# Performance work log

Hardware: AMD Instinct MI355X
Metric: run time of the kernel (lower is better)

The kernel has to match this reference:

```python
import jax, jax.numpy as jnp
import numpy as np

T = 10       # Newton-Schulz iterations (module init arg)
EPS = 1e-05  # ridge added to covariance


def setup_inputs() -> dict:
    key = jax.random.key(0)
    # [B, C, H, W] feature map fed into the concept-whitening layer
    X = jax.random.normal(key, (128, 256, 28, 28), dtype=jnp.float32)
    return {"X": X}


def _iternorm_whiten(X):
    """Training-mode IterNorm whitening (g=1 group): ZCA via Newton-Schulz."""
    B, C, H, W = X.shape
    # X.transpose(0,1).view(C, -1): channels-first flatten -> [C, m], m = B*H*W
    x = jnp.moveaxis(X, 0, 1).reshape(C, -1)
    m = x.shape[-1]
    mean = x.mean(-1, keepdims=True)                      # [C, 1]
    xc = x - mean                                         # [C, m]
    I = jnp.eye(C, dtype=X.dtype)
    # Sigma = eps*I + (1/m) * xc @ xc^T
    Sigma = EPS * I + (xc @ xc.T) * (1.0 / m)             # [C, C]
    rTr = 1.0 / jnp.trace(Sigma)                          # scalar
    Sigma_N = Sigma * rTr                                 # trace-normalized

    def newton_step(P, _):
        # P_{k+1} = 1.5*P_k - 0.5 * P_k^3 @ Sigma_N
        P3 = P @ P @ P
        return 1.5 * P - 0.5 * (P3 @ Sigma_N), None

    P, _ = jax.lax.scan(newton_step, I, None, length=T)
    wm = P * jnp.sqrt(rTr)                                # whitening matrix [C, C]
    xn = wm @ xc                                          # [C, m]
    # reshape back: view(C, B, H, W).transpose(0, 1) -> [B, C, H, W]
    return jnp.moveaxis(xn.reshape(C, B, H, W), 0, 1)


def reference(X):
    # IterNormRotation.forward with mode=-1 (default): X_hat = IterNorm.apply(X, ...)
    # The concept-alignment branch (mode >= 0) runs under no_grad and is skipped.
    return _iternorm_whiten(X)
```

## Files before the change

kernel.cpp:

```cpp
#include <hip/hip_runtime.h>


#define HW 784
#define BHW 200704
#define INV_M (1.0f/100352.0f)
#define EPS_RIDGE 1e-5f

typedef __bf16 bf8 __attribute__((ext_vector_type(8)));
typedef float  f4  __attribute__((ext_vector_type(4)));

__device__ __forceinline__ f4 mfma16(bf8 a, bf8 b, f4 c){
  return __builtin_amdgcn_mfma_f32_16x16x32_bf16(a, b, c, 0, 0, 0);
}

__device__ __forceinline__ unsigned short f2bf_rne(float f){
  unsigned u = __builtin_bit_cast(unsigned, f);
  return (unsigned short)((u + 0x7fffu + ((u >> 16) & 1u)) >> 16);
}
__device__ __forceinline__ float bf2f(unsigned short h){
  unsigned u = ((unsigned)h) << 16;
  return __builtin_bit_cast(float, u);
}
__device__ __forceinline__ void split_bf(float f, unsigned short& h, unsigned short& l){
  h = f2bf_rne(f);
  float r = f - bf2f(h);
  l = f2bf_rne(r);
}

__global__ __launch_bounds__(512, 2) void cov_kernel(const float* __restrict__ X,
                                                     float* __restrict__ part,
                                                     float* __restrict__ chansum){
  __shared__ unsigned short Ah[256][40];
  __shared__ unsigned short Al[256][40];
  __shared__ float ssum[256];
  const int t = threadIdx.x;
  const int blk = blockIdx.x;
  const int b = blk >> 1;
  const int h = blk & 1;
  const int base_hw = h * 400;
  const int len    = h ? 384 : 400;
  const int nsteps = h ? 12  : 13;
  const float* __restrict__ Xb = X + (size_t)b * BHW;

  if (t < 256) ssum[t] = 0.0f;

  const int lane = t & 63;
  const int wave = t >> 6;
  const int wm = wave >> 2;
  const int wn = wave & 3;
  const int lr = lane & 15;
  const int ko = lane >> 4;

  f4 acc[8][4];
  #pragma unroll
  for (int m = 0; m < 8; m++)
    #pragma unroll
    for (int n = 0; n < 4; n++) acc[m][n] = f4{0.f, 0.f, 0.f, 0.f};

  float csum[4] = {0.f, 0.f, 0.f, 0.f};
  const int srow = t >> 3;
  const int sfq  = t & 7;

  for (int ks = 0; ks < nsteps; ++ks){
    if (ks) __syncthreads();
    #pragma unroll
    for (int i = 0; i < 4; i++){
      int row = srow + i * 64;
      int hwl = ks * 32 + sfq * 4;
      float4 v = make_float4(0.f, 0.f, 0.f, 0.f);
      if (hwl < len) v = *(const float4*)&Xb[(size_t)row * HW + base_hw + hwl];
      csum[i] += v.x + v.y + v.z + v.w;
      unsigned short h0,l0,h1,l1,h2,l2,h3,l3;
      split_bf(v.x, h0, l0); split_bf(v.y, h1, l1);
      split_bf(v.z, h2, l2); split_bf(v.w, h3, l3);
      *(ushort4*)&Ah[row][sfq * 4] = make_ushort4(h0, h1, h2, h3);
      *(ushort4*)&Al[row][sfq * 4] = make_ushort4(l0, l1, l2, l3);
    }
    __syncthreads();
    bf8 bhf[4], blf[4];
    #pragma unroll
    for (int n = 0; n < 4; n++){
      int coln = wn * 64 + n * 16 + lr;
      bhf[n] = *(const bf8*)&Ah[coln][ko * 8];
      blf[n] = *(const bf8*)&Al[coln][ko * 8];
    }
    #pragma unroll
    for (int m = 0; m < 8; m++){
      int rowm = wm * 128 + m * 16 + lr;
      bf8 ahf = *(const bf8*)&Ah[rowm][ko * 8];
      bf8 alf = *(const bf8*)&Al[rowm][ko * 8];
      #pragma unroll
      for (int n = 0; n < 4; n++){
        acc[m][n] = mfma16(ahf, bhf[n], acc[m][n]);
        acc[m][n] = mfma16(ahf, blf[n], acc[m][n]);
        acc[m][n] = mfma16(alf, bhf[n], acc[m][n]);
      }
    }
  }
  atomicAdd(&ssum[srow      ], csum[0]);
  atomicAdd(&ssum[srow +  64], csum[1]);
  atomicAdd(&ssum[srow + 128], csum[2]);
  atomicAdd(&ssum[srow + 192], csum[3]);
  __syncthreads();
  if (t < 256) atomicAdd(&chansum[t], ssum[t]);

  float* __restrict__ Pp = part + (size_t)blk * 65536;
  const int cr4 = (lane >> 4) * 4;
  #pragma unroll
  for (int m = 0; m < 8; m++){
    #pragma unroll
    for (int n = 0; n < 4; n++){
      int colw = wn * 64 + n * 16 + lr;
      #pragma unroll
      for (int r = 0; r < 4; r++){
        int roww = wm * 128 + m * 16 + cr4 + r;
        Pp[roww * 256 + colw] = acc[m][n][r];
      }
    }
  }
}

__global__ __launch_bounds__(256) void reduce_kernel(const float* __restrict__ part,
                                                     const float* __restrict__ chansum,
                                                     float* __restrict__ Sig,
                                                     float* __restrict__ trace){
  const int i = blockIdx.x;
  const int j = threadIdx.x;
  float s = 0.f;
  #pragma unroll 8
  for (int p = 0; p < 256; p++) s += part[(size_t)p * 65536 + i * 256 + j];
  float mi = chansum[i] * INV_M;
  float mj = chansum[j] * INV_M;
  float v = s * INV_M - mi * mj + ((i == j) ? EPS_RIDGE : 0.f);
  Sig[i * 256 + j] = v;
  if (i == j) atomicAdd(trace, v);
}

__global__ __launch_bounds__(256) void prep_kernel(const float* __restrict__ Sig,
                                                   const float* __restrict__ trace,
                                                   float* __restrict__ SigN,
                                                   float* __restrict__ P1){
  const int idx = blockIdx.x * 256 + threadIdx.x;
  const float rTr = 1.0f / trace[0];
  const float sn = Sig[idx] * rTr;
  SigN[idx] = sn;
  const int i = idx >> 8, j = idx & 255;
  P1[idx] = ((i == j) ? 1.5f : 0.0f) - 0.5f * sn;
}

__global__ __launch_bounds__(256) void ns64_kernel(const float* __restrict__ A,
                                                   const float* __restrict__ B0,
                                                   const float* __restrict__ B1,
                                                   float* __restrict__ O0,
                                                   float* __restrict__ O1,
                                                   const float* __restrict__ E,
                                                   float alpha, float beta){
  const float* __restrict__ B = blockIdx.z ? B1 : B0;
  float* __restrict__ O = blockIdx.z ? O1 : O0;
  __shared__ unsigned short Ah[64][136], Al[64][136], Bh[64][136], Bl[64][136];
  const int t = threadIdx.x;
  const int lane = t & 63;
  const int wave = t >> 6;
  const int wm = wave >> 1, wn = wave & 1;
  const int lr = lane & 15, ko = lane >> 4;
  const int r0 = blockIdx.x * 64, c0 = blockIdx.y * 64;
  const int srow = t >> 2;
  const int sc0 = (t & 3) * 32;
  f4 acc[2][2];
  acc[0][0] = f4{0.f,0.f,0.f,0.f}; acc[0][1] = f4{0.f,0.f,0.f,0.f};
  acc[1][0] = f4{0.f,0.f,0.f,0.f}; acc[1][1] = f4{0.f,0.f,0.f,0.f};

  for (int kh = 0; kh < 2; ++kh){
    if (kh) __syncthreads();
    #pragma unroll
    for (int i = 0; i < 8; i++){
      int col = sc0 + i * 4;
      int gcol = kh * 128 + col;
      unsigned short h0,l0,h1,l1,h2,l2,h3,l3;
      float4 va = *(const float4*)&A[(r0 + srow) * 256 + gcol];
      split_bf(va.x,h0,l0); split_bf(va.y,h1,l1); split_bf(va.z,h2,l2); split_bf(va.w,h3,l3);
      *(ushort4*)&Ah[srow][col] = make_ushort4(h0,h1,h2,h3);
      *(ushort4*)&Al[srow][col] = make_ushort4(l0,l1,l2,l3);
      float4 vb = *(const float4*)&B[(c0 + srow) * 256 + gcol];
      split_bf(vb.x,h0,l0); split_bf(vb.y,h1,l1); split_bf(vb.z,h2,l2); split_bf(vb.w,h3,l3);
      *(ushort4*)&Bh[srow][col] = make_ushort4(h0,h1,h2,h3);
      *(ushort4*)&Bl[srow][col] = make_ushort4(l0,l1,l2,l3);
    }
    __syncthreads();
    #pragma unroll
    for (int ks = 0; ks < 4; ++ks){
      #pragma unroll
      for (int m = 0; m < 2; m++){
        bf8 ahf = *(const bf8*)&Ah[wm * 32 + m * 16 + lr][ks * 32 + ko * 8];
        bf8 alf = *(const bf8*)&Al[wm * 32 + m * 16 + lr][ks * 32 + ko * 8];
        #pragma unroll
        for (int n = 0; n < 2; n++){
          bf8 bhf = *(const bf8*)&Bh[wn * 32 + n * 16 + lr][ks * 32 + ko * 8];
          bf8 blf = *(const bf8*)&Bl[wn * 32 + n * 16 + lr][ks * 32 + ko * 8];
          acc[m][n] = mfma16(ahf, bhf, acc[m][n]);
          acc[m][n] = mfma16(ahf, blf, acc[m][n]);
          acc[m][n] = mfma16(alf, bhf, acc[m][n]);
        }
      }
    }
  }
  const int cr4 = (lane >> 4) * 4;
  #pragma unroll
  for (int m = 0; m < 2; m++)
    #pragma unroll
    for (int n = 0; n < 2; n++)
      #pragma unroll
      for (int r = 0; r < 4; r++){
        int row = r0 + wm * 32 + m * 16 + cr4 + r;
        int col = c0 + wn * 32 + n * 16 + lr;
        float v = alpha * acc[m][n][r];
        if (beta != 0.0f) v += beta * E[row * 256 + col];
        O[row * 256 + col] = v;
      }
}

__global__ __launch_bounds__(256) void wmprep_kernel(const float* __restrict__ P,
                                                     const float* __restrict__ trace,
                                                     const float* __restrict__ chansum,
                                                     unsigned short* __restrict__ wmhi,
                                                     unsigned short* __restrict__ wmlo,
                                                     float* __restrict__ woff){
  const int i = blockIdx.x, t = threadIdx.x;
  __shared__ float red[256];
  const float s = sqrtf(1.0f / trace[0]);
  float v = P[i * 256 + t] * s;
  unsigned short h, l;
  split_bf(v, h, l);
  wmhi[i * 256 + t] = h;
  wmlo[i * 256 + t] = l;
  red[t] = v * (chansum[t] * INV_M);
  __syncthreads();
  for (int st = 128; st > 0; st >>= 1){
    if (t < st) red[t] += red[t + st];
    __syncthreads();
  }
  if (t == 0) woff[i] = red[0];
}

__global__ __launch_bounds__(512, 2) void whiten_kernel(const float* __restrict__ X,
                                                        const unsigned short* __restrict__ wmhi,
                                                        const unsigned short* __restrict__ wmlo,
                                                        const float* __restrict__ woff,
                                                        float* __restrict__ out){
  __shared__ unsigned short Ahs[256][40], Als[256][40];
  __shared__ unsigned short Bhs[112][40], Bls[112][40];
  const int blk = blockIdx.x;
  const int b = blk / 7;
  const int ch = blk % 7;
  const int hw0 = ch * 112;
  const int t = threadIdx.x;
  const int lane = t & 63;
  const int wave = t >> 6;
  const int lr = lane & 15, ko = lane >> 4;
  const float* __restrict__ Xb = X + (size_t)b * BHW;
  f4 acc[2][7];
  #pragma unroll
  for (int m = 0; m < 2; m++)
    #pragma unroll
    for (int n = 0; n < 7; n++) acc[m][n] = f4{0.f, 0.f, 0.f, 0.f};

  const int arow = t >> 1, aseg = t & 1;
  const int g = lane >> 4;
  const int cc = (t >> 4);
  for (int ks = 0; ks < 8; ++ks){
    if (ks) __syncthreads();
    {
      const uint4* sh = (const uint4*)(wmhi + arow * 256 + ks * 32 + aseg * 16);
      uint4 v0 = sh[0], v1 = sh[1];
      *(uint4*)&Ahs[arow][aseg * 16]     = v0;
      *(uint4*)&Ahs[arow][aseg * 16 + 8] = v1;
      const uint4* sl = (const uint4*)(wmlo + arow * 256 + ks * 32 + aseg * 16);
      uint4 w0 = sl[0], w1 = sl[1];
      *(uint4*)&Als[arow][aseg * 16]     = w0;
      *(uint4*)&Als[arow][aseg * 16 + 8] = w1;
    }
    #pragma unroll
    for (int p = 0; p < 2; p++){
      int qh = p * 16 + (t & 15);
      if (qh < 28){
        float4 v = *(const float4*)&Xb[(size_t)(ks * 32 + cc) * HW + hw0 + qh * 4];
        float r0 = __shfl_xor((g & 1) ? v.x : v.y, 16);
        float r1 = __shfl_xor((g & 1) ? v.z : v.w, 16);
        float a0 = (g & 1) ? r0  : v.x;
        float a1 = (g & 1) ? v.y : r0;
        float a2 = (g & 1) ? r1  : v.z;
        float a3 = (g & 1) ? v.w : r1;
        float s0 = __shfl_xor((g & 2) ? a0 : a2, 32);
        float s1 = __shfl_xor((g & 2) ? a1 : a3, 32);
        float b0v = (g & 2) ? s0 : a0;
        float b1v = (g & 2) ? s1 : a1;
        float b2v = (g & 2) ? a2 : s0;
        float b3v = (g & 2) ? a3 : s1;
        int row = qh * 4 + g;
        int colk = (t >> 6) * 4;
        unsigned short h0,l0,h1,l1,h2,l2,h3,l3;
        split_bf(b0v,h0,l0); split_bf(b1v,h1,l1); split_bf(b2v,h2,l2); split_bf(b3v,h3,l3);
        *(ushort4*)&Bhs[row][colk] = make_ushort4(h0,h1,h2,h3);
        *(ushort4*)&Bls[row][colk] = make_ushort4(l0,l1,l2,l3);
      }
    }
    __syncthreads();
    bf8 bhf[7], blf[7];
    #pragma unroll
    for (int n = 0; n < 7; n++){
      bhf[n] = *(const bf8*)&Bhs[n * 16 + lr][ko * 8];
      blf[n] = *(const bf8*)&Bls[n * 16 + lr][ko * 8];
    }
    #pragma unroll
    for (int m = 0; m < 2; m++){
      bf8 ahf = *(const bf8*)&Ahs[wave * 32 + m * 16 + lr][ko * 8];
      bf8 alf = *(const bf8*)&Als[wave * 32 + m * 16 + lr][ko * 8];
      #pragma unroll
      for (int n = 0; n < 7; n++){
        acc[m][n] = mfma16(ahf, bhf[n], acc[m][n]);
        acc[m][n] = mfma16(ahf, blf[n], acc[m][n]);
        acc[m][n] = mfma16(alf, bhf[n], acc[m][n]);
      }
    }
  }
  const int cr4 = (lane >> 4) * 4;
  #pragma unroll
  for (int m = 0; m < 2; m++){
    #pragma unroll
    for (int r = 0; r < 4; r++){
      int c = wave * 32 + m * 16 + cr4 + r;
      float wofc = woff[c];
      #pragma unroll
      for (int n = 0; n < 7; n++){
        int hw = hw0 + n * 16 + lr;
        out[(size_t)b * BHW + (size_t)c * HW + hw] = acc[m][n][r] - wofc;
      }
    }
  }
}

extern "C" void kernel_launch(void* const* d_in, const int* in_sizes, int n_in,
                              void* d_out, int out_size, void* d_ws, size_t ws_size,
                              hipStream_t stream){
  const float* X = (const float*)d_in[0];
  float* out = (float*)d_out;
  char* ws = (char*)d_ws;
  float* part    = (float*)(ws);
  float* chansum = (float*)(ws + 67108864);
  float* trace   = (float*)(ws + 67108864 + 1024);
  float* Sig     = (float*)(ws + 67110912);
  float* SigN    = (float*)(ws + 67373056);
  float* Pa      = (float*)(ws + 67635200);
  float* Pb      = (float*)(ws + 67897344);
  float* C1      = (float*)(ws + 68159488);
  float* C2      = (float*)(ws + 68421632);
  float* woff    = (float*)(ws + 68683776);
  unsigned short* wmhi = (unsigned short*)(ws + 68685824);
  unsigned short* wmlo = (unsigned short*)(ws + 68816896);

  hipMemsetAsync(ws + 67108864, 0, 2048, stream);
  cov_kernel   <<<256, 512, 0, stream>>>(X, part, chansum);
  reduce_kernel<<<256, 256, 0, stream>>>(part, chansum, Sig, trace);
  prep_kernel  <<<256, 256, 0, stream>>>(Sig, trace, SigN, Pa);

  float* P = Pa; float* Pn = Pb;
  for (int it = 0; it < 9; ++it){
    ns64_kernel<<<dim3(4,4,2), 256, 0, stream>>>(P, P, SigN, C1, C2, nullptr, 1.0f, 0.0f);
    ns64_kernel<<<dim3(4,4,1), 256, 0, stream>>>(C1, C2, nullptr, Pn, nullptr, P, -0.5f, 1.5f);
    float* tmp = P; P = Pn; Pn = tmp;
  }

  wmprep_kernel<<<256, 256, 0, stream>>>(P, trace, chansum, wmhi, wmlo, woff);
  whiten_kernel<<<896, 512, 0, stream>>>(X, wmhi, wmlo, woff, out);
}
```

Measured before the change: 495.8 us.

## Fuse Newton-Schulz iterations into one cooperative kernel and swizzle whiten LDS

Replaces the prep, the 18 per-iteration ns64 launches and the wmprep launch with a single cooperative kernel of 32 blocks that uses grid.sync between matrix-multiply stages. This removes roughly 20 kernel launches and the gaps between them on the small 256x256 iteration chain. Separately, it XOR-swizzles the B-tile column layout in the whiten kernel's LDS to reduce bank conflicts. The costs are grid-wide barrier overhead, low parallelism with only 32 blocks, and half of the blocks sitting idle during the second multiply of each iteration.

```diff
diff --git a/kernel.cpp b/kernel.cpp
--- a/kernel.cpp
+++ b/kernel.cpp
@@ -1,4 +1,7 @@
 #include <hip/hip_runtime.h>
+#include <hip/hip_cooperative_groups.h>
+
+namespace cg = cooperative_groups;
 
 
 #define HW 784
@@ -136,34 +139,20 @@
   if (i == j) atomicAdd(trace, v);
 }
 
-__global__ __launch_bounds__(256) void prep_kernel(const float* __restrict__ Sig,
-                                                   const float* __restrict__ trace,
-                                                   float* __restrict__ SigN,
-                                                   float* __restrict__ P1){
-  const int idx = blockIdx.x * 256 + threadIdx.x;
-  const float rTr = 1.0f / trace[0];
-  const float sn = Sig[idx] * rTr;
-  SigN[idx] = sn;
-  const int i = idx >> 8, j = idx & 255;
-  P1[idx] = ((i == j) ? 1.5f : 0.0f) - 0.5f * sn;
-}
-
-__global__ __launch_bounds__(256) void ns64_kernel(const float* __restrict__ A,
-                                                   const float* __restrict__ B0,
-                                                   const float* __restrict__ B1,
-                                                   float* __restrict__ O0,
-                                                   float* __restrict__ O1,
-                                                   const float* __restrict__ E,
-                                                   float alpha, float beta){
-  const float* __restrict__ B = blockIdx.z ? B1 : B0;
-  float* __restrict__ O = blockIdx.z ? O1 : O0;
-  __shared__ unsigned short Ah[64][136], Al[64][136], Bh[64][136], Bl[64][136];
-  const int t = threadIdx.x;
+typedef unsigned short lds64_t[64][136];
+
+__device__ __forceinline__ void mm_tile64(const float* __restrict__ A,
+                                          const float* __restrict__ B,
+                                          float* __restrict__ O,
+                                          const float* __restrict__ E,
+                                          float alpha, float beta,
+                                          int r0, int c0, int t,
+                                          lds64_t& Ah, lds64_t& Al,
+                                          lds64_t& Bh, lds64_t& Bl){
   const int lane = t & 63;
   const int wave = t >> 6;
   const int wm = wave >> 1, wn = wave & 1;
   const int lr = lane & 15, ko = lane >> 4;
-  const int r0 = blockIdx.x * 64, c0 = blockIdx.y * 64;
   const int srow = t >> 2;
   const int sc0 = (t & 3) * 32;
   f4 acc[2][2];
@@ -219,27 +208,67 @@
       }
 }
 
-__global__ __launch_bounds__(256) void wmprep_kernel(const float* __restrict__ P,
-                                                     const float* __restrict__ trace,
-                                                     const float* __restrict__ chansum,
-                                                     unsigned short* __restrict__ wmhi,
-                                                     unsigned short* __restrict__ wmlo,
-                                                     float* __restrict__ woff){
-  const int i = blockIdx.x, t = threadIdx.x;
+__global__ __launch_bounds__(256) void nsfused_kernel(const float* __restrict__ Sig,
+                                                      const float* __restrict__ trace,
+                                                      const float* __restrict__ chansum,
+                                                      float* __restrict__ SigN,
+                                                      float* Pa, float* Pb,
+                                                      float* __restrict__ C1,
+                                                      float* __restrict__ C2,
+                                                      unsigned short* __restrict__ wmhi,
+                                                      unsigned short* __restrict__ wmlo,
+                                                      float* __restrict__ woff){
+  cg::grid_group grid = cg::this_grid();
+  __shared__ lds64_t Ah, Al, Bh, Bl;
   __shared__ float red[256];
-  const float s = sqrtf(1.0f / trace[0]);
-  float v = P[i * 256 + t] * s;
-  unsigned short h, l;
-  split_bf(v, h, l);
-  wmhi[i * 256 + t] = h;
-  wmlo[i * 256 + t] = l;
-  red[t] = v * (chansum[t] * INV_M);
-  __syncthreads();
-  for (int st = 128; st > 0; st >>= 1){
-    if (t < st) red[t] += red[t + st];
+  const int t = threadIdx.x;
+  const int blk = blockIdx.x;
+  const float rTr = 1.0f / trace[0];
+
+  #pragma unroll
+  for (int i = 0; i < 8; i++){
+    int idx = (blk * 8 + i) * 256 + t;
+    float sn = Sig[idx] * rTr;
+    SigN[idx] = sn;
+    int r = idx >> 8, c = idx & 255;
+    Pa[idx] = ((r == c) ? 1.5f : 0.0f) - 0.5f * sn;
+  }
+  grid.sync();
+
+  float* P  = Pa;
+  float* Pn = Pb;
+  const int job = blk & 15;
+  const int r0 = (job >> 2) * 64, c0 = (job & 3) * 64;
+  for (int it = 0; it < 9; ++it){
+    {
+      const float* Bmat = (blk < 16) ? (const float*)P : SigN;
+      float* Omat = (blk < 16) ? C1 : C2;
+      mm_tile64(P, Bmat, Omat, nullptr, 1.0f, 0.0f, r0, c0, t, Ah, Al, Bh, Bl);
+    }
+    grid.sync();
+    if (blk < 16)
+      mm_tile64(C1, C2, Pn, P, -0.5f, 1.5f, r0, c0, t, Ah, Al, Bh, Bl);
+    grid.sync();
+    float* tmp = P; P = Pn; Pn = tmp;
+  }
+
+  const float s = sqrtf(rTr);
+  for (int r8 = 0; r8 < 8; ++r8){
+    int i = blk * 8 + r8;
+    float v = P[i * 256 + t] * s;
+    unsigned short h, l;
+    split_bf(v, h, l);
+    wmhi[i * 256 + t] = h;
+    wmlo[i * 256 + t] = l;
+    red[t] = v * (chansum[t] * INV_M);
     __syncthreads();
-  }
-  if (t == 0) woff[i] = red[0];
+    for (int st = 128; st > 0; st >>= 1){
+      if (t < st) red[t] += red[t + st];
+      __syncthreads();
+    }
+    if (t == 0) woff[i] = red[0];
+    __syncthreads();
+  }
 }
 
 __global__ __launch_bounds__(512, 2) void whiten_kernel(const float* __restrict__ X,
@@ -267,6 +296,7 @@
   const int arow = t >> 1, aseg = t & 1;
   const int g = lane >> 4;
   const int cc = (t >> 4);
+  const int pko = ko ^ ((lr >> 2) & 3);
   for (int ks = 0; ks < 8; ++ks){
     if (ks) __syncthreads();
     {
@@ -297,7 +327,8 @@
         float b2v = (g & 2) ? a2 : s0;
         float b3v = (g & 2) ? a3 : s1;
         int row = qh * 4 + g;
-        int colk = (t >> 6) * 4;
+        int w = t >> 6;
+        int colk = (((w >> 1) ^ (qh & 3)) << 3) + (w & 1) * 4;
         unsigned short h0,l0,h1,l1,h2,l2,h3,l3;
         split_bf(b0v,h0,l0); split_bf(b1v,h1,l1); split_bf(b2v,h2,l2); split_bf(b3v,h3,l3);
         *(ushort4*)&Bhs[row][colk] = make_ushort4(h0,h1,h2,h3);
@@ -308,8 +339,8 @@
     bf8 bhf[7], blf[7];
     #pragma unroll
     for (int n = 0; n < 7; n++){
-      bhf[n] = *(const bf8*)&Bhs[n * 16 + lr][ko * 8];
-      blf[n] = *(const bf8*)&Bls[n * 16 + lr][ko * 8];
+      bhf[n] = *(const bf8*)&Bhs[n * 16 + lr][pko * 8];
+      blf[n] = *(const bf8*)&Bls[n * 16 + lr][pko * 8];
     }
     #pragma unroll
     for (int m = 0; m < 2; m++){
@@ -361,15 +392,20 @@
   hipMemsetAsync(ws + 67108864, 0, 2048, stream);
   cov_kernel   <<<256, 512, 0, stream>>>(X, part, chansum);
   reduce_kernel<<<256, 256, 0, stream>>>(part, chansum, Sig, trace);
-  prep_kernel  <<<256, 256, 0, stream>>>(Sig, trace, SigN, Pa);
-
-  float* P = Pa; float* Pn = Pb;
-  for (int it = 0; it < 9; ++it){
-    ns64_kernel<<<dim3(4,4,2), 256, 0, stream>>>(P, P, SigN, C1, C2, nullptr, 1.0f, 0.0f);
-    ns64_kernel<<<dim3(4,4,1), 256, 0, stream>>>(C1, C2, nullptr, Pn, nullptr, P, -0.5f, 1.5f);
-    float* tmp = P; P = Pn; Pn = tmp;
-  }
-
-  wmprep_kernel<<<256, 256, 0, stream>>>(P, trace, chansum, wmhi, wmlo, woff);
+
+  const float* Sig_c = Sig;
+  const float* trace_c = trace;
+  const float* chansum_c = chansum;
+  float* SigN_p = SigN; float* Pa_p = Pa; float* Pb_p = Pb;
+  float* C1_p = C1; float* C2_p = C2;
+  unsigned short* wmhi_p = wmhi; unsigned short* wmlo_p = wmlo;
+  float* woff_p = woff;
+  void* kargs[] = {(void*)&Sig_c, (void*)&trace_c, (void*)&chansum_c,
+                   (void*)&SigN_p, (void*)&Pa_p, (void*)&Pb_p,
+                   (void*)&C1_p, (void*)&C2_p,
+                   (void*)&wmhi_p, (void*)&wmlo_p, (void*)&woff_p};
+  hipLaunchCooperativeKernel((void*)nsfused_kernel, dim3(32), dim3(256),
+                             kargs, 0, stream);
+
   whiten_kernel<<<896, 512, 0, stream>>>(X, wmhi, wmlo, woff, out);
 }
```

After: 567.2 us. 1.14x slower.
